# Performance work log

Hardware: AMD Instinct MI355X
Metric: run time of the kernel (lower is better)

Reference implementation:

```python
import jax, jax.numpy as jnp
import numpy as np

N_NODES = 50000
N_EDGES = 800000
IN_CH = 64
OUT_CH = 32
HEADS = 4
NUM_EDGE_TYPES = 64


def _sincos_pe(max_len, d_model):
    pos = np.arange(max_len, dtype=np.float32)[:, None]
    div = np.exp(np.arange(0, d_model, 2, dtype=np.float32) * (-np.log(10000.0) / d_model))
    pe = np.zeros((max_len, d_model), dtype=np.float32)
    pe[:, 0::2] = np.sin(pos * div)
    pe[:, 1::2] = np.cos(pos * div)
    return jnp.asarray(pe)


def setup_inputs() -> dict:
    key = jax.random.key(0)
    k1, k2, k3, k4, k5, k6 = jax.random.split(key, 6)
    x = jax.random.uniform(k1, (N_NODES, IN_CH), dtype=jnp.float32)
    edge_index = jax.random.randint(k2, (2, N_EDGES), 0, N_NODES, dtype=jnp.int64)
    edge_type = jax.random.randint(k3, (N_EDGES,), 0, NUM_EDGE_TYPES, dtype=jnp.int64)
    pe = _sincos_pe(NUM_EDGE_TYPES, IN_CH)
    W = jax.random.normal(k4, (IN_CH, HEADS * OUT_CH), dtype=jnp.float32) * 0.1
    att_src = jax.random.normal(k5, (HEADS, OUT_CH), dtype=jnp.float32) * 0.1
    att_dst = jax.random.normal(k6, (HEADS, OUT_CH), dtype=jnp.float32) * 0.1
    bias = jnp.zeros((HEADS * OUT_CH,), dtype=jnp.float32)
    return {"x": x, "edge_index": edge_index, "edge_type": edge_type, "pe": pe,
            "W": W, "att_src": att_src, "att_dst": att_dst, "bias": bias}


def reference(x, edge_index, edge_type, pe, W, att_src, att_dst, bias):
    N = x.shape[0]
    H, C = att_src.shape
    src, dst = edge_index[0], edge_index[1]

    # edge-wise positional encoding scatter-added into source nodes
    x_pos = x.at[src].add(pe[edge_type])

    # GATConv (PyG defaults: add_self_loops=True, negative_slope=0.2, concat=True)
    xl = (x_pos @ W).reshape(N, H, C)              # [N, H, C]
    a_src = (xl * att_src[None]).sum(-1)           # [N, H]
    a_dst = (xl * att_dst[None]).sum(-1)           # [N, H]

    self_idx = jnp.arange(N)
    src2 = jnp.concatenate([src, self_idx])        # [E'] with self loops
    dst2 = jnp.concatenate([dst, self_idx])

    alpha = jax.nn.leaky_relu(a_src[src2] + a_dst[dst2], 0.2)   # [E', H]
    amax = jax.ops.segment_max(alpha, dst2, num_segments=N)     # per-target max
    ex = jnp.exp(alpha - amax[dst2])
    denom = jax.ops.segment_sum(ex, dst2, num_segments=N)
    coef = ex / denom[dst2]                                     # segment softmax

    out = jax.ops.segment_sum(coef[:, :, None] * xl[src2], dst2, num_segments=N)
    out = out.reshape(N, H * C) + bias
    return jax.nn.elu(out)
```

## Files before the change

kernel.cpp:

```cpp
#include <hip/hip_runtime.h>
#include <cstdint>
#include <cstddef>

#define N_NODES 50000
#define N_EDGES 800000
#define IN_CH   64
#define OC      128
#define HEADS   4
#define CH      32

#define NB      391
#define BCAP    2560
#define EPB     2048
#define HIST_BLOCKS ((N_EDGES + EPB - 1) / EPB)

#define SENTINEL N_NODES
#define LST_LEN  (N_EDGES + 4 * N_NODES)

typedef __attribute__((ext_vector_type(8))) short short8;
typedef __attribute__((ext_vector_type(4))) float f32x4;

static inline int ceil_div(int a, int b){ return (a + b - 1) / b; }

__device__ __forceinline__ float lrelu(float x){ return fmaxf(x, 0.2f * x); }

__device__ __forceinline__ float bf_lo(unsigned u){ return __uint_as_float(u << 16); }
__device__ __forceinline__ float bf_hi(unsigned u){ return __uint_as_float(u & 0xFFFF0000u); }

__device__ __forceinline__ unsigned pack_bf16(float x, float y){
  unsigned ux = __float_as_uint(x), uy = __float_as_uint(y);
  ux += 0x7FFFu + ((ux >> 16) & 1u);
  uy += 0x7FFFu + ((uy >> 16) & 1u);
  return (ux >> 16) | (uy & 0xFFFF0000u);
}

__global__ __launch_bounds__(256) void k_hist_prep(const int* __restrict__ ei,
                                                   const int* __restrict__ et,
                                                   const float* __restrict__ pe,
                                                   const float* __restrict__ W,
                                                   unsigned* __restrict__ Bh,
                                                   int* __restrict__ btail,
                                                   unsigned* __restrict__ bbuf,
                                                   float* __restrict__ a_src,
                                                   unsigned* __restrict__ xh,
                                                   unsigned short* __restrict__ lst){
  __shared__ __align__(16) char smem[26816];
  int tid = threadIdx.x;

  if (blockIdx.x < HIST_BLOCKS){
    int* cnt  = (int*)smem;
    int* lofs = cnt + 784;
    int* gpos = lofs + 784;
    unsigned* stage = (unsigned*)(gpos + 784);
    int* sred = (int*)(stage + 4096);

    for (int i = tid; i < 784; i += 256) cnt[i] = 0;
    __syncthreads();

    int e0 = blockIdx.x * EPB;
    unsigned ent[16];
    int rnk[16];
    short bck[16];
    #pragma unroll
    for (int j = 0; j < 8; ++j){
      int e = e0 + j * 256 + tid;
      bck[2 * j] = -1; bck[2 * j + 1] = -1;
      if (e < N_EDGES){
        int s = ei[e], d = ei[N_EDGES + e], t = et[e];
        int bd = d >> 7, bs = s >> 7;
        ent[2 * j]     = ((unsigned)bd << 23) | ((unsigned)(d & 127) << 16) | (unsigned)s;
        ent[2 * j + 1] = ((unsigned)bs << 23) | ((unsigned)(s & 127) << 16) | (unsigned)t;
        bck[2 * j]     = (short)bd;
        bck[2 * j + 1] = (short)(391 + bs);
        rnk[2 * j]     = atomicAdd(&cnt[bd], 1);
        rnk[2 * j + 1] = atomicAdd(&cnt[391 + bs], 1);
      }
    }
    __syncthreads();

    int v[4], pre[4], run = 0;
    #pragma unroll
    for (int i = 0; i < 4; ++i){
      int idx = tid * 4 + i;
      v[i] = (idx < 784) ? cnt[idx] : 0;
      pre[i] = run; run += v[i];
    }
    sred[tid] = run; __syncthreads();
    for (int off = 1; off < 256; off <<= 1){
      int t = (tid >= off) ? sred[tid - off] : 0;
      __syncthreads();
      sred[tid] += t;
      __syncthreads();
    }
    int toff = sred[tid] - run;
    #pragma unroll
    for (int i = 0; i < 4; ++i){
      int idx = tid * 4 + i;
      if (idx < 784) lofs[idx] = toff + pre[i];
    }
    __syncthreads();

    #pragma unroll
    for (int j = 0; j < 16; ++j){
      if (bck[j] >= 0) stage[lofs[bck[j]] + rnk[j]] = ent[j];
    }
    for (int b = tid; b < 782; b += 256){
      int c = cnt[b];
      gpos[b] = c ? atomicAdd(&btail[b], c) : 0;
    }
    __syncthreads();

    int totalD = lofs[391];
    int totalA = lofs[782];
    for (int i = tid; i < totalA; i += 256){
      unsigned e = stage[i];
      int b9 = (int)(e >> 23);
      int bc = (i < totalD) ? b9 : 391 + b9;
      int gp = gpos[bc] + (i - lofs[bc]);
      if (gp < BCAP) bbuf[(size_t)bc * BCAP + gp] = e;
    }
  } else {
    float* sPe  = (float*)smem;
    float* sW64 = sPe + 4096;
    float* sPeW = sW64 + 1024;
    int nt = blockIdx.x - HIST_BLOCKS;
    int n0 = nt * 16;
    if (nt == 0){
      if (tid < 64) xh[(size_t)SENTINEL * 64 + tid] = 0;
      if (tid < 4)  a_src[SENTINEL * 4 + tid] = -1e30f;
      if (tid < 32) lst[LST_LEN + tid] = (unsigned short)SENTINEL;
    }
    for (int i = tid; i < 1024; i += 256)
      ((float4*)sPe)[i] = ((const float4*)pe)[i];
    for (int i = tid; i < 1024; i += 256){
      int k = i >> 4, j = i & 15;
      sW64[i] = W[k * 128 + n0 + j];
    }
    __syncthreads();
    for (int i = tid; i < 1024; i += 256){
      int t = i >> 4, j = i & 15;
      float a = 0.f;
      #pragma unroll
      for (int k = 0; k < 64; ++k) a += sPe[t * 64 + k] * sW64[k * 16 + j];
      sPeW[i] = a;
    }
    __syncthreads();
    for (int m = tid; m < 1024; m += 256){
      int j2 = m & 3, l = (m >> 2) & 63, kk = m >> 8;
      int k = kk * 32 + (l >> 4) * 8 + 2 * j2;
      int jl = l & 15;
      float v0, v1;
      if (k < 64){ v0 = sW64[k * 16 + jl]; v1 = sW64[(k + 1) * 16 + jl]; }
      else       { v0 = sPeW[(k - 64) * 16 + jl]; v1 = sPeW[(k - 63) * 16 + jl]; }
      Bh[nt * 1024 + m] = pack_bf16(v0, v1);
    }
  }
}

__global__ __launch_bounds__(256) void k_passB(const unsigned* __restrict__ bbuf,
                                               const int* __restrict__ btail,
                                               int* __restrict__ row_dst,
                                               unsigned short* __restrict__ lst,
                                               const float* __restrict__ x,
                                               const unsigned* __restrict__ Bh,
                                               const float* __restrict__ att_s,
                                               const float* __restrict__ att_d,
                                               float* __restrict__ a_src,
                                               float* __restrict__ a_dst,
                                               unsigned* __restrict__ xh){
  int g = blockIdx.x, tid = threadIdx.x;
  if (g < NB){
    __shared__ int cnt[128], sc[128], cur[128], red[256];
    __shared__ int sbase;
    int d0 = g << 7;
    int nn = min(128, N_NODES - d0);
    int cnt_b = min(btail[g], BCAP);
    int part = 0;
    for (int q = tid; q < g; q += 256) part += min(btail[q], BCAP);
    red[tid] = part; __syncthreads();
    for (int off = 128; off > 0; off >>= 1){
      if (tid < off) red[tid] += red[tid + off];
      __syncthreads();
    }
    if (tid == 0) sbase = red[0];
    if (tid < 128) cnt[tid] = 0;
    __syncthreads();
    int base0 = sbase + 4 * d0;
    for (int i = tid; i < cnt_b; i += 256)
      atomicAdd(&cnt[(bbuf[(size_t)g * BCAP + i] >> 16) & 127], 1);
    __syncthreads();
    if (tid < 128) sc[tid] = cnt[tid];
    __syncthreads();
    for (int off = 1; off < 128; off <<= 1){
      int t = (tid < 128 && tid >= off) ? sc[tid - off] : 0;
      __syncthreads();
      if (tid < 128) sc[tid] += t;
      __syncthreads();
    }
    if (tid < nn){
      int ex = sc[tid] - cnt[tid];
      cur[tid] = ex + 4 * tid;
      row_dst[d0 + tid] = base0 + ex + 4 * tid;
    }
    if (g == NB - 1 && tid == 0) row_dst[N_NODES] = base0 + cnt_b + 4 * nn;
    __syncthreads();
    for (int i = tid; i < cnt_b; i += 256){
      unsigned e = bbuf[(size_t)g * BCAP + i];
      int p = atomicAdd(&cur[(e >> 16) & 127], 1);
      lst[base0 + p] = (unsigned short)(e & 0xFFFFu);
    }
    __syncthreads();
    if (tid < nn){
      int pe_ = cur[tid];
      #pragma unroll
      for (int k = 0; k < 4; ++k) lst[base0 + pe_ + k] = (unsigned short)SENTINEL;
    }
  } else {
    __shared__ unsigned hist[128 * 16];
    __shared__ unsigned sB[8192];
    __shared__ unsigned sA[4096];
    int n0 = (g - NB) << 7;
    for (int i = tid; i < 2048; i += 256) hist[i] = 0;
    __syncthreads();
    int cnt_b = min(btail[g], BCAP);
    for (int i = tid; i < cnt_b; i += 256){
      unsigned e = bbuf[(size_t)g * BCAP + i];
      unsigned t = e & 63u;
      atomicAdd(&hist[((e >> 16) & 127) * 16 + (t >> 2)], 1u << (8 * (t & 3)));
    }
    {
      const uint4* srcp = (const uint4*)Bh;
      uint4* dstp = (uint4*)sB;
      #pragma unroll
      for (int i = 0; i < 8; ++i) dstp[tid + i * 256] = srcp[tid + i * 256];
    }
    __syncthreads();

    int wid = tid >> 6, l = tid & 63;
    int c15 = l & 15, kq = l >> 4;
    float asv[8], adv[8];
    #pragma unroll
    for (int nt = 0; nt < 8; ++nt){
      asv[nt] = att_s[nt * 16 + c15];
      adv[nt] = att_d[nt * 16 + c15];
    }

    for (int half = 0; half < 2; ++half){
      int row0 = n0 + half * 64;
      {
        int r = tid >> 2, q = tid & 3;
        int n = row0 + r;
        unsigned swz = (unsigned)((r & 7) << 4);
        float4 xv[4];
        if (n < N_NODES){
          const float4* xr = (const float4*)(x + (size_t)n * 64);
          #pragma unroll
          for (int i = 0; i < 4; ++i) xv[i] = xr[q * 4 + i];
        } else {
          #pragma unroll
          for (int i = 0; i < 4; ++i) xv[i] = make_float4(0.f, 0.f, 0.f, 0.f);
        }
        unsigned pk[8];
        #pragma unroll
        for (int i = 0; i < 4; ++i){
          pk[2 * i]     = pack_bf16(xv[i].x, xv[i].y);
          pk[2 * i + 1] = pack_bf16(xv[i].z, xv[i].w);
        }
        unsigned b0 = (unsigned)(r * 256 + q * 32);
        *(uint4*)(sA + (((b0)      ^ swz) >> 2)) = make_uint4(pk[0], pk[1], pk[2], pk[3]);
        *(uint4*)(sA + (((b0 + 16) ^ swz) >> 2)) = make_uint4(pk[4], pk[5], pk[6], pk[7]);
        unsigned cw[4];
        #pragma unroll
        for (int i = 0; i < 4; ++i) cw[i] = hist[(half * 64 + r) * 16 + q * 4 + i];
        unsigned pc[8];
        #pragma unroll
        for (int i = 0; i < 4; ++i){
          unsigned w = cw[i];
          pc[2 * i]     = pack_bf16((float)(w & 0xFFu), (float)((w >> 8) & 0xFFu));
          pc[2 * i + 1] = pack_bf16((float)((w >> 16) & 0xFFu), (float)(w >> 24));
        }
        unsigned b1 = (unsigned)(r * 256 + 128 + q * 32);
        *(uint4*)(sA + (((b1)      ^ swz) >> 2)) = make_uint4(pc[0], pc[1], pc[2], pc[3]);
        *(uint4*)(sA + (((b1 + 16) ^ swz) >> 2)) = make_uint4(pc[4], pc[5], pc[6], pc[7]);
      }
      __syncthreads();

      int arow = wid * 16 + c15;
      f32x4 acc[8];
      #pragma unroll
      for (int nt = 0; nt < 8; ++nt) acc[nt] = (f32x4){0.f, 0.f, 0.f, 0.f};
      #pragma unroll
      for (int kk = 0; kk < 4; ++kk){
        unsigned abyte = (unsigned)(arow * 256 + kk * 64 + kq * 16);
        abyte ^= (unsigned)((arow & 7) << 4);
        short8 af = *(const short8*)((const char*)sA + abyte);
        #pragma unroll
        for (int nt = 0; nt < 8; ++nt){
          short8 bf = *(const short8*)(sB + (size_t)((nt * 4 + kk) * 64 + l) * 4);
          acc[nt] = __builtin_amdgcn_mfma_f32_16x16x32_bf16(af, bf, acc[nt], 0, 0, 0);
        }
      }

      #pragma unroll
      for (int r = 0; r < 4; ++r){
        int row = row0 + wid * 16 + kq * 4 + r;
        bool valid = row < N_NODES;
        #pragma unroll
        for (int h = 0; h < 4; ++h){
          float ps = acc[2 * h][r] * asv[2 * h] + acc[2 * h + 1][r] * asv[2 * h + 1];
          float pd = acc[2 * h][r] * adv[2 * h] + acc[2 * h + 1][r] * adv[2 * h + 1];
          #pragma unroll
          for (int m = 1; m < 16; m <<= 1){
            ps += __shfl_xor(ps, m);
            pd += __shfl_xor(pd, m);
          }
          if (valid && c15 == 0){
            a_src[row * 4 + h] = ps;
            a_dst[row * 4 + h] = pd;
          }
        }
        #pragma unroll
        for (int nt = 0; nt < 8; ++nt){
          float own = acc[nt][r];
          float nb = __shfl_xor(own, 1);
          if (valid && !(c15 & 1))
            xh[(size_t)row * 64 + nt * 8 + (c15 >> 1)] = pack_bf16(own, nb);
        }
      }
      __syncthreads();
    }
  }
}

__global__ __launch_bounds__(256) void k_aggregate(const int* __restrict__ row_dst,
                                                   const unsigned short* __restrict__ lst,
                                                   const float* __restrict__ a_src,
                                                   const float* __restrict__ a_dst,
                                                   const unsigned* __restrict__ xh,
                                                   const float* __restrict__ bias,
                                                   float* __restrict__ out){
  int n = (blockIdx.x * blockDim.x + threadIdx.x) >> 6;
  if (n >= N_NODES) return;
  int l = threadIdx.x & 63;
  int h = l >> 4;
  float ad = a_dst[n * 4 + h];

  float w = __expf(lrelu(a_src[n * 4 + h] + ad));
  unsigned uv = xh[(size_t)n * 64 + l];
  float l0 = w, l1 = 0.f, l2 = 0.f, l3 = 0.f;
  float a0x = w * bf_lo(uv), a0y = w * bf_hi(uv);
  float a1x = 0.f, a1y = 0.f, a2x = 0.f, a2y = 0.f, a3x = 0.f, a3y = 0.f;

  int k0 = row_dst[n];
  int k1 = row_dst[n + 1] - 4;

  #define LOADB(U0,B0,U1,B1,U2,B2,U3,B3, base) {                          \
    int t0 = (int)lst[(base)],     t1 = (int)lst[(base) + 1];             \
    int t2 = (int)lst[(base) + 2], t3 = (int)lst[(base) + 3];             \
    U0 = xh[(size_t)t0 * 64 + l];  B0 = a_src[t0 * 4 + h];                \
    U1 = xh[(size_t)t1 * 64 + l];  B1 = a_src[t1 * 4 + h];                \
    U2 = xh[(size_t)t2 * 64 + l];  B2 = a_src[t2 * 4 + h];                \
    U3 = xh[(size_t)t3 * 64 + l];  B3 = a_src[t3 * 4 + h];                \
  }
  #define PROC4(U0,B0,U1,B1,U2,B2,U3,B3) {                                \
    float w0 = __expf(lrelu(B0 + ad));                                    \
    l0 += w0; a0x = fmaf(w0, bf_lo(U0), a0x); a0y = fmaf(w0, bf_hi(U0), a0y); \
    float w1 = __expf(lrelu(B1 + ad));                                    \
    l1 += w1; a1x = fmaf(w1, bf_lo(U1), a1x); a1y = fmaf(w1, bf_hi(U1), a1y); \
    float w2 = __expf(lrelu(B2 + ad));                                    \
    l2 += w2; a2x = fmaf(w2, bf_lo(U2), a2x); a2y = fmaf(w2, bf_hi(U2), a2y); \
    float w3 = __expf(lrelu(B3 + ad));                                    \
    l3 += w3; a3x = fmaf(w3, bf_lo(U3), a3x); a3y = fmaf(w3, bf_hi(U3), a3y); \
  }

  unsigned uA0, uA1, uA2, uA3, uB0, uB1, uB2, uB3, n0_, n1_, n2_, n3_;
  float bA0, bA1, bA2, bA3, bB0, bB1, bB2, bB3, f0_, f1_, f2_, f3_;

  if (k0 < k1){
    int j = k0;
    LOADB(uA0,bA0, uA1,bA1, uA2,bA2, uA3,bA3, j);
    LOADB(uB0,bB0, uB1,bB1, uB2,bB2, uB3,bB3, j + 4);
    for (;;){
      LOADB(n0_,f0_, n1_,f1_, n2_,f2_, n3_,f3_, j + 8);
      PROC4(uA0,bA0, uA1,bA1, uA2,bA2, uA3,bA3);
      uA0 = n0_; bA0 = f0_; uA1 = n1_; bA1 = f1_;
      uA2 = n2_; bA2 = f2_; uA3 = n3_; bA3 = f3_;
      j += 4;
      if (j >= k1) break;
      LOADB(n0_,f0_, n1_,f1_, n2_,f2_, n3_,f3_, j + 8);
      PROC4(uB0,bB0, uB1,bB1, uB2,bB2, uB3,bB3);
      uB0 = n0_; bB0 = f0_; uB1 = n1_; bB1 = f1_;
      uB2 = n2_; bB2 = f2_; uB3 = n3_; bB3 = f3_;
      j += 4;
      if (j >= k1) break;
    }
  }
  #undef LOADB
  #undef PROC4

  float lsum = (l0 + l1) + (l2 + l3);
  float accx = (a0x + a1x) + (a2x + a3x);
  float accy = (a0y + a1y) + (a2y + a3y);
  float2 b = ((const float2*)bias)[l];
  float r0 = accx / lsum + b.x;
  float r1 = accy / lsum + b.y;
  float2 o;
  o.x = r0 > 0.f ? r0 : expm1f(r0);
  o.y = r1 > 0.f ? r1 : expm1f(r1);
  ((float2*)out)[(size_t)n * 64 + l] = o;
}

extern "C" void kernel_launch(void* const* d_in, const int* in_sizes, int n_in,
                              void* d_out, int out_size, void* d_ws, size_t ws_size,
                              hipStream_t stream){
  const float* x     = (const float*)d_in[0];
  const int*   ei    = (const int*)d_in[1];
  const int*   et    = (const int*)d_in[2];
  const float* pe    = (const float*)d_in[3];
  const float* W     = (const float*)d_in[4];
  const float* att_s = (const float*)d_in[5];
  const float* att_d = (const float*)d_in[6];
  const float* bias  = (const float*)d_in[7];
  float* out = (float*)d_out;

  int*      btail   = (int*)d_ws;
  int*      row_dst = btail + 1024;
  unsigned* Bh      = (unsigned*)(row_dst + N_NODES + 8);
  float*    a_src   = (float*)(Bh + 8192);
  float*    a_dst   = a_src + (size_t)(N_NODES + 1) * 4;
  unsigned* xh      = (unsigned*)(a_dst + (size_t)N_NODES * 4);
  unsigned* bbuf    = xh + (size_t)(N_NODES + 1) * 64;
  unsigned short* lst = (unsigned short*)(bbuf + (size_t)2 * NB * BCAP);

  const int B = 256;

  hipMemsetAsync(btail, 0, 1024 * sizeof(int), stream);
  k_hist_prep<<<HIST_BLOCKS + 8, B, 0, stream>>>(ei, et, pe, W, Bh, btail, bbuf,
                                                 a_src, xh, lst);
  k_passB<<<2 * NB, B, 0, stream>>>(bbuf, btail, row_dst, lst,
                                    x, Bh, att_s, att_d, a_src, a_dst, xh);
  k_aggregate<<<ceil_div(N_NODES * 64, B), B, 0, stream>>>(row_dst, lst, a_src, a_dst,
                                                           xh, bias, out);
}
```

Measured before the change: 101.2 us.

## Split bf16 feature table per head and gather four edges per wavefront

Stores the bf16 projected features head-major (four separate tables of 16 packed words per node) rather than node-major with 64 words. The aggregate kernel loops over heads, and each wavefront's four 16-lane slots handle different edges in parallel, then reduce with cross-slot shuffles. The goal is smaller per-edge gathers with better locality in each head table, keeping more edges in flight per wavefront. In exchange, each thread runs four sequential head passes with extra shuffles, reloads the edge list four times, and leaves three quarters of the lanes idle during the output write.

```diff
diff --git a/kernel.cpp b/kernel.cpp
--- a/kernel.cpp
+++ b/kernel.cpp
@@ -126,7 +126,8 @@
     int nt = blockIdx.x - HIST_BLOCKS;
     int n0 = nt * 16;
     if (nt == 0){
-      if (tid < 64) xh[(size_t)SENTINEL * 64 + tid] = 0;
+      if (tid < 64)
+        xh[((size_t)(tid >> 4) * (N_NODES + 1) + SENTINEL) * 16 + (tid & 15)] = 0;
       if (tid < 4)  a_src[SENTINEL * 4 + tid] = -1e30f;
       if (tid < 32) lst[LST_LEN + tid] = (unsigned short)SENTINEL;
     }
@@ -323,8 +324,11 @@
         for (int nt = 0; nt < 8; ++nt){
           float own = acc[nt][r];
           float nb = __shfl_xor(own, 1);
-          if (valid && !(c15 & 1))
-            xh[(size_t)row * 64 + nt * 8 + (c15 >> 1)] = pack_bf16(own, nb);
+          if (valid && !(c15 & 1)){
+            int hh = nt >> 1;
+            int pair = (nt & 1) * 8 + (c15 >> 1);
+            xh[((size_t)hh * (N_NODES + 1) + row) * 16 + pair] = pack_bf16(own, nb);
+          }
         }
       }
       __syncthreads();
@@ -342,72 +346,82 @@
   int n = (blockIdx.x * blockDim.x + threadIdx.x) >> 6;
   if (n >= N_NODES) return;
   int l = threadIdx.x & 63;
-  int h = l >> 4;
-  float ad = a_dst[n * 4 + h];
-
-  float w = __expf(lrelu(a_src[n * 4 + h] + ad));
-  unsigned uv = xh[(size_t)n * 64 + l];
-  float l0 = w, l1 = 0.f, l2 = 0.f, l3 = 0.f;
-  float a0x = w * bf_lo(uv), a0y = w * bf_hi(uv);
-  float a1x = 0.f, a1y = 0.f, a2x = 0.f, a2y = 0.f, a3x = 0.f, a3y = 0.f;
+  int slot = l >> 4;
+  int c = l & 15;
 
   int k0 = row_dst[n];
   int k1 = row_dst[n + 1] - 4;
 
-  #define LOADB(U0,B0,U1,B1,U2,B2,U3,B3, base) {                          \
-    int t0 = (int)lst[(base)],     t1 = (int)lst[(base) + 1];             \
-    int t2 = (int)lst[(base) + 2], t3 = (int)lst[(base) + 3];             \
-    U0 = xh[(size_t)t0 * 64 + l];  B0 = a_src[t0 * 4 + h];                \
-    U1 = xh[(size_t)t1 * 64 + l];  B1 = a_src[t1 * 4 + h];                \
-    U2 = xh[(size_t)t2 * 64 + l];  B2 = a_src[t2 * 4 + h];                \
-    U3 = xh[(size_t)t3 * 64 + l];  B3 = a_src[t3 * 4 + h];                \
+  float4 ad4 = *(const float4*)(a_dst + (size_t)n * 4);
+  float4 as4 = *(const float4*)(a_src + (size_t)n * 4);
+  float advs[4] = {ad4.x, ad4.y, ad4.z, ad4.w};
+  float asvs[4] = {as4.x, as4.y, as4.z, as4.w};
+
+  #pragma unroll
+  for (int h = 0; h < 4; ++h){
+    const unsigned* T = xh + (size_t)h * (N_NODES + 1) * 16;
+    float ad = advs[h];
+
+    float wself = __expf(lrelu(asvs[h] + ad));
+    unsigned uv = T[(size_t)n * 16 + c];
+    float lp = 0.f, ax = 0.f, ay = 0.f;
+    if (slot == 0){
+      lp = wself;
+      ax = wself * bf_lo(uv);
+      ay = wself * bf_hi(uv);
+    }
+
+    #define LOADG(U, B, base) {                     \
+      int t_ = (int)lst[(base) + slot];             \
+      U = T[(size_t)t_ * 16 + c];                   \
+      B = a_src[t_ * 4 + h]; }
+    #define PROCG(U, B) {                           \
+      float w_ = __expf(lrelu((B) + ad));           \
+      lp += w_;                                     \
+      ax = fmaf(w_, bf_lo(U), ax);                  \
+      ay = fmaf(w_, bf_hi(U), ay); }
+
+    if (k0 < k1){
+      unsigned u0 = 0, u1 = 0, u2 = 0, u3 = 0;
+      float b0 = -1e30f, b1 = -1e30f, b2 = -1e30f, b3 = -1e30f;
+      int j = k0;
+      LOADG(u0, b0, j);
+      if (j + 4  < k1) LOADG(u1, b1, j + 4);
+      if (j + 8  < k1) LOADG(u2, b2, j + 8);
+      if (j + 12 < k1) LOADG(u3, b3, j + 12);
+      for (;;){
+        PROCG(u0, b0);
+        j += 4; if (j >= k1) break;
+        if (j + 12 < k1) LOADG(u0, b0, j + 12);
+        PROCG(u1, b1);
+        j += 4; if (j >= k1) break;
+        if (j + 12 < k1) LOADG(u1, b1, j + 12);
+        PROCG(u2, b2);
+        j += 4; if (j >= k1) break;
+        if (j + 12 < k1) LOADG(u2, b2, j + 12);
+        PROCG(u3, b3);
+        j += 4; if (j >= k1) break;
+        if (j + 12 < k1) LOADG(u3, b3, j + 12);
+      }
+    }
+    #undef LOADG
+    #undef PROCG
+
+    lp += __shfl_xor(lp, 16); lp += __shfl_xor(lp, 32);
+    ax += __shfl_xor(ax, 16); ax += __shfl_xor(ax, 32);
+    ay += __shfl_xor(ay, 16); ay += __shfl_xor(ay, 32);
+
+    if (slot == 0){
+      float inv = 1.f / lp;
+      float2 bb = ((const float2*)bias)[h * 16 + c];
+      float r0 = ax * inv + bb.x;
+      float r1 = ay * inv + bb.y;
+      float2 o;
+      o.x = r0 > 0.f ? r0 : expm1f(r0);
+      o.y = r1 > 0.f ? r1 : expm1f(r1);
+      ((float2*)out)[(size_t)n * 64 + h * 16 + c] = o;
+    }
   }
-  #define PROC4(U0,B0,U1,B1,U2,B2,U3,B3) {                                \
-    float w0 = __expf(lrelu(B0 + ad));                                    \
-    l0 += w0; a0x = fmaf(w0, bf_lo(U0), a0x); a0y = fmaf(w0, bf_hi(U0), a0y); \
-    float w1 = __expf(lrelu(B1 + ad));                                    \
-    l1 += w1; a1x = fmaf(w1, bf_lo(U1), a1x); a1y = fmaf(w1, bf_hi(U1), a1y); \
-    float w2 = __expf(lrelu(B2 + ad));                                    \
-    l2 += w2; a2x = fmaf(w2, bf_lo(U2), a2x); a2y = fmaf(w2, bf_hi(U2), a2y); \
-    float w3 = __expf(lrelu(B3 + ad));                                    \
-    l3 += w3; a3x = fmaf(w3, bf_lo(U3), a3x); a3y = fmaf(w3, bf_hi(U3), a3y); \
-  }
-
-  unsigned uA0, uA1, uA2, uA3, uB0, uB1, uB2, uB3, n0_, n1_, n2_, n3_;
-  float bA0, bA1, bA2, bA3, bB0, bB1, bB2, bB3, f0_, f1_, f2_, f3_;
-
-  if (k0 < k1){
-    int j = k0;
-    LOADB(uA0,bA0, uA1,bA1, uA2,bA2, uA3,bA3, j);
-    LOADB(uB0,bB0, uB1,bB1, uB2,bB2, uB3,bB3, j + 4);
-    for (;;){
-      LOADB(n0_,f0_, n1_,f1_, n2_,f2_, n3_,f3_, j + 8);
-      PROC4(uA0,bA0, uA1,bA1, uA2,bA2, uA3,bA3);
-      uA0 = n0_; bA0 = f0_; uA1 = n1_; bA1 = f1_;
-      uA2 = n2_; bA2 = f2_; uA3 = n3_; bA3 = f3_;
-      j += 4;
-      if (j >= k1) break;
-      LOADB(n0_,f0_, n1_,f1_, n2_,f2_, n3_,f3_, j + 8);
-      PROC4(uB0,bB0, uB1,bB1, uB2,bB2, uB3,bB3);
-      uB0 = n0_; bB0 = f0_; uB1 = n1_; bB1 = f1_;
-      uB2 = n2_; bB2 = f2_; uB3 = n3_; bB3 = f3_;
-      j += 4;
-      if (j >= k1) break;
-    }
-  }
-  #undef LOADB
-  #undef PROC4
-
-  float lsum = (l0 + l1) + (l2 + l3);
-  float accx = (a0x + a1x) + (a2x + a3x);
-  float accy = (a0y + a1y) + (a2y + a3y);
-  float2 b = ((const float2*)bias)[l];
-  float r0 = accx / lsum + b.x;
-  float r1 = accy / lsum + b.y;
-  float2 o;
-  o.x = r0 > 0.f ? r0 : expm1f(r0);
-  o.y = r1 > 0.f ? r1 : expm1f(r1);
-  ((float2*)out)[(size_t)n * 64 + l] = o;
 }
 
 extern "C" void kernel_launch(void* const* d_in, const int* in_sizes, int n_in,
@@ -429,7 +443,7 @@
   float*    a_src   = (float*)(Bh + 8192);
   float*    a_dst   = a_src + (size_t)(N_NODES + 1) * 4;
   unsigned* xh      = (unsigned*)(a_dst + (size_t)N_NODES * 4);
-  unsigned* bbuf    = xh + (size_t)(N_NODES + 1) * 64;
+  unsigned* bbuf    = xh + (size_t)4 * (N_NODES + 1) * 16;
   unsigned short* lst = (unsigned short*)(bbuf + (size_t)2 * NB * BCAP);
 
   const int B = 256;
```

Result: slower. 157.2 us (+55.3%).
